# Kernel optimization log

Measured on AMD Instinct MI355X. Metric: run time of the kernel, lower is better.

## Reference

```python
import jax, jax.numpy as jnp
import numpy as np

LMAX, MMAX = 4, 2
K = (LMAX + 1) ** 2                                 # 25 SH coefficients (l-major node layout)
NL = [LMAX - m + 1 for m in range(MMAX + 1)]        # coeffs per order m: [5,4,3]
M_COEFF = NL[0] + sum(2 * n for n in NL[1:])        # 19 coeffs in m-major (mmax-truncated) edge layout
SPHERE_C, HIDDEN_C = 64, 64
NUM_HEADS, ALPHA_C, VALUE_C, OUT_C = 8, 32, 16, 64
P_GRID = 100
N_NODES, N_EDGES = 4096, 24576
NUM_SPECIES, EDGE_C, EMB_C = 90, 64, 64
N_EXTRA = NUM_HEADS * ALPHA_C + HIDDEN_C            # extra m=0 channels for S2_SEP: alpha + gate scalars


def _ln(x, g, b, eps=1e-5):
    mu = jnp.mean(x, -1, keepdims=True)
    var = jnp.var(x, -1, keepdims=True)
    return (x - mu) * jax.lax.rsqrt(var + eps) * g + b


def _smooth_leaky_relu(x, neg=0.2):
    return 0.5 * (1.0 + neg) * x + 0.5 * (1.0 - neg) * x * (2.0 * jax.nn.sigmoid(x) - 1.0)


def _segment_softmax(a, seg, n):
    amax = jax.lax.stop_gradient(jax.ops.segment_max(a, seg, num_segments=n))
    amax = jnp.where(jnp.isfinite(amax), amax, 0.0)
    e = jnp.exp(a - amax[seg])
    s = jax.ops.segment_sum(e, seg, num_segments=n)
    return e / (s[seg] + 1e-16)


def _so2_conv(x, w0, b0, wms, c_in, c_out, x_edge=None, n_extra=0):
    # x: [E, M_COEFF, c_in] in m-major layout (m=0 block, then per m: real rows then imag rows)
    E = x.shape[0]
    L0 = NL[0]
    x0 = x[:, :L0, :].reshape(E, L0 * c_in)
    if x_edge is not None:
        x0 = x0 * x_edge[:, :L0 * c_in]
    y0 = x0 @ w0 + b0
    extra = None
    if n_extra:
        extra = y0[:, L0 * c_out:]
        y0 = y0[:, :L0 * c_out]
    outs = [y0.reshape(E, L0, c_out)]
    off, rad = L0, L0 * c_in
    for m in range(1, MMAX + 1):
        nl = NL[m]
        xr = x[:, off:off + nl, :]
        xi = x[:, off + nl:off + 2 * nl, :]
        if x_edge is not None:
            s = x_edge[:, rad:rad + nl * c_in].reshape(E, nl, c_in)
            xr, xi = xr * s, xi * s
        xr = xr.reshape(E, nl * c_in)
        xi = xi.reshape(E, nl * c_in)
        half = nl * c_out
        wa, wb = wms[m - 1][:, :half], wms[m - 1][:, half:]
        yr = (xr @ wa - xi @ wb).reshape(E, nl, c_out)  # complex block-matmul
        yi = (xr @ wb + xi @ wa).reshape(E, nl, c_out)
        outs.append(jnp.concatenate([yr, yi], axis=1))
        off += 2 * nl
        rad += nl * c_in
    return jnp.concatenate(outs, axis=1), extra


def setup_inputs():
    key = jax.random.key(0)
    ks = iter(jax.random.split(key, 48))
    def w(shape, fan_in):
        return jax.random.normal(next(ks), shape, jnp.float32) / np.sqrt(fan_in)
    inp = {}
    inp['node_feats'] = jax.random.normal(next(ks), (N_NODES, K, SPHERE_C), jnp.float32)
    inp['node_species'] = jax.random.randint(next(ks), (N_NODES,), 0, NUM_SPECIES)
    inp['edge_distances'] = jax.random.normal(next(ks), (N_EDGES, EDGE_C), jnp.float32)
    inp['senders'] = jax.random.randint(next(ks), (N_EDGES,), 0, N_NODES)
    inp['receivers'] = jax.random.randint(next(ks), (N_EDGES,), 0, N_NODES)
    inp['wigner'] = jax.random.normal(next(ks), (N_EDGES, M_COEFF, K), jnp.float32) / np.sqrt(K)
    inp['snd_emb'] = jax.random.normal(next(ks), (NUM_SPECIES, EMB_C), jnp.float32) * 0.001
    inp['rcv_emb'] = jax.random.normal(next(ks), (NUM_SPECIES, EMB_C), jnp.float32) * 0.001
    ec = EDGE_C + 2 * EMB_C                              # 192 after atom-edge embedding concat
    n_rad = 2 * SPHERE_C * (NL[0] + NL[1] + NL[2])       # 1536 per-edge scales for conv1
    inp['rad_w1'] = w((ec, 64), ec); inp['rad_b1'] = jnp.zeros((64,))
    inp['rad_g1'] = jnp.ones((64,)); inp['rad_be1'] = jnp.zeros((64,))
    inp['rad_w2'] = w((64, 64), 64); inp['rad_b2'] = jnp.zeros((64,))
    inp['rad_g2'] = jnp.ones((64,)); inp['rad_be2'] = jnp.zeros((64,))
    inp['rad_w3'] = w((64, n_rad), 64); inp['rad_b3'] = jnp.ones((n_rad,))
    cin1 = 2 * SPHERE_C
    inp['c1_w0'] = w((NL[0] * cin1, NL[0] * HIDDEN_C + N_EXTRA), NL[0] * cin1)
    inp['c1_b0'] = jnp.zeros((NL[0] * HIDDEN_C + N_EXTRA,))
    inp['c1_wm1'] = w((NL[1] * cin1, 2 * NL[1] * HIDDEN_C), NL[1] * cin1)
    inp['c1_wm2'] = w((NL[2] * cin1, 2 * NL[2] * HIDDEN_C), NL[2] * cin1)
    inp['aln_g'] = jnp.ones((ALPHA_C,)); inp['aln_b'] = jnp.zeros((ALPHA_C,))
    inp['alpha_dot'] = w((NUM_HEADS, ALPHA_C), ALPHA_C)
    inp['to_grid'] = jax.random.normal(next(ks), (P_GRID, M_COEFF), jnp.float32) / np.sqrt(M_COEFF)
    inp['from_grid'] = jax.random.normal(next(ks), (M_COEFF, P_GRID), jnp.float32) / np.sqrt(P_GRID)
    cv = NUM_HEADS * VALUE_C
    inp['c2_w0'] = w((NL[0] * HIDDEN_C, NL[0] * cv), NL[0] * HIDDEN_C)
    inp['c2_b0'] = jnp.zeros((NL[0] * cv,))
    inp['c2_wm1'] = w((NL[1] * HIDDEN_C, 2 * NL[1] * cv), NL[1] * HIDDEN_C)
    inp['c2_wm2'] = w((NL[2] * HIDDEN_C, 2 * NL[2] * cv), NL[2] * HIDDEN_C)
    inp['proj_w'] = w((LMAX + 1, cv, OUT_C), cv)
    inp['proj_b'] = jnp.zeros((OUT_C,))
    return inp


def reference(node_feats, node_species, edge_distances, senders, receivers, wigner,
              snd_emb, rcv_emb, rad_w1, rad_b1, rad_g1, rad_be1, rad_w2, rad_b2,
              rad_g2, rad_be2, rad_w3, rad_b3, c1_w0, c1_b0, c1_wm1, c1_wm2,
              aln_g, aln_b, alpha_dot, to_grid, from_grid,
              c2_w0, c2_b0, c2_wm1, c2_wm2, proj_w, proj_b):
    N = node_feats.shape[0]
    # atom-edge embedding gathers + concat with radial-basis distances
    edge_embeds = jnp.concatenate([edge_distances,
                                   snd_emb[node_species[senders]],
                                   rcv_emb[node_species[receivers]]], axis=1)
    msgs = jnp.concatenate([node_feats[senders], node_feats[receivers]], axis=2)  # [E,25,128]
    msgs = jnp.einsum('emk,ekc->emc', wigner, msgs)                               # rotate to edge frame [E,19,128]
    # radial function -> per-edge input scales for SO2 conv 1
    h = jax.nn.silu(_ln(edge_embeds @ rad_w1 + rad_b1, rad_g1, rad_be1))
    h = jax.nn.silu(_ln(h @ rad_w2 + rad_b2, rad_g2, rad_be2))
    x_edge = h @ rad_w3 + rad_b3
    msgs, x0_extra = _so2_conv(msgs, c1_w0, c1_b0, [c1_wm1, c1_wm2],
                               2 * SPHERE_C, HIDDEN_C, x_edge, N_EXTRA)
    x0_alpha = x0_extra[:, :NUM_HEADS * ALPHA_C]
    x0_gate = x0_extra[:, NUM_HEADS * ALPHA_C:]
    # separable S2 activation: SiLU on sphere grid for l>0, SiLU on scalars for l=0
    grid = jax.nn.silu(jnp.einsum('pm,emc->epc', to_grid, msgs))
    tens = jnp.einsum('mp,epc->emc', from_grid, grid)
    msgs = jnp.concatenate([jax.nn.silu(x0_gate)[:, None, :], tens[:, 1:, :]], axis=1)
    msgs, _ = _so2_conv(msgs, c2_w0, c2_b0, [c2_wm1, c2_wm2], HIDDEN_C, NUM_HEADS * VALUE_C)
    # attention weights: LN -> SmoothLeakyReLU -> dot -> per-receiver softmax
    a = _smooth_leaky_relu(_ln(x0_alpha.reshape(-1, NUM_HEADS, ALPHA_C), aln_g, aln_b))
    alpha = _segment_softmax(jnp.einsum('ehk,hk->eh', a, alpha_dot), receivers, N)
    attn = msgs.reshape(-1, M_COEFF, NUM_HEADS, VALUE_C) * alpha[:, None, :, None]
    msgs = attn.reshape(-1, M_COEFF, NUM_HEADS * VALUE_C)
    msgs = jnp.einsum('emk,emc->ekc', wigner, msgs)    # rotate back (W^T), [E,25,128]
    node = jax.ops.segment_sum(msgs, receivers, num_segments=N)
    # SO3 linear: per-degree-l channel mixing, bias only on l=0
    l_of_k = jnp.asarray(np.repeat(np.arange(LMAX + 1), 2 * np.arange(LMAX + 1) + 1))
    out = jnp.einsum('nkc,kcd->nkd', node, proj_w[l_of_k])
    return out.at[:, 0, :].add(proj_b)
```

## Files before the change

### kernel.cpp

```cpp
#include <hip/hip_runtime.h>

typedef unsigned short u16;
typedef unsigned int u32;
typedef __attribute__((ext_vector_type(8))) short short8;
typedef __attribute__((ext_vector_type(4))) float floatx4;

#define E_EDGES 24576
#define EC 12288
#define N_NODES_C 4096

__device__ __forceinline__ float bf2f(u16 u) {
    union { u32 i; float f; } v; v.i = ((u32)u) << 16; return v.f;
}
__device__ __forceinline__ u16 f2bf(float f) {
    union { float f; u32 i; } v; v.f = f;
    u32 x = v.i;
    u32 r = (x + 0x7fffu + ((x >> 16) & 1u)) >> 16;
    return (u16)r;
}
__device__ __forceinline__ u32 pk_bf16(float a, float b) {
    u32 r;
    asm("v_cvt_pk_bf16_f32 %0, %1, %2" : "=v"(r) : "v"(a), "v"(b));
    return r;
}
__device__ __forceinline__ u32 encf(float f) {
    union { float f; u32 i; } v; v.f = f;
    return (v.i & 0x80000000u) ? ~v.i : (v.i | 0x80000000u);
}
__device__ __forceinline__ float decf(u32 u) {
    union { u32 i; float f; } v;
    v.i = (u & 0x80000000u) ? (u ^ 0x80000000u) : ~u;
    return v.f;
}
__device__ __forceinline__ float sigmoidf_(float x) { return __fdividef(1.f, 1.f + __expf(-x)); }
__device__ __forceinline__ float siluf_(float x) { return x * __fdividef(1.f, 1.f + __expf(-x)); }

__device__ __forceinline__ void gld16(const u16* g, u16* l) {
    __builtin_amdgcn_global_load_lds((const __attribute__((address_space(1))) unsigned int*)g,
                                     (__attribute__((address_space(3))) unsigned int*)l, 16, 0, 0);
}

__global__ void k_diag(float* __restrict__ out, int n) {
    int i = blockIdx.x * 256 + threadIdx.x;
    if (i < n) out[i] = 1000.0f;
}

__global__ void k_transpose(const float* __restrict__ src, u16* __restrict__ dst, int K, int N) {
    int idx = blockIdx.x * 256 + threadIdx.x;
    if (idx >= K * N) return;
    int k = idx / N, n = idx % N;
    dst[n * K + k] = f2bf(src[idx]);
}
__global__ void k_combine(const float* __restrict__ src, u16* __restrict__ dst, int K, int H) {
    int total = 4 * K * H;
    int idx = blockIdx.x * 256 + threadIdx.x;
    if (idx >= total) return;
    int n = idx / (2 * K), k = idx % (2 * K);
    float v;
    if (k < K) v = src[k * 2 * H + n];
    else {
        int kk = k - K;
        if (n < H) v = -src[kk * 2 * H + H + n];
        else       v = src[kk * 2 * H + (n - H)];
    }
    dst[idx] = f2bf(v);
}

__global__ void k_packgrid(const float* __restrict__ tg, const float* __restrict__ fg,
                           u16* __restrict__ tgP, u16* __restrict__ fgP) {
    int idx = blockIdx.x * 256 + threadIdx.x;
    if (idx < 112 * 32) {
        int p = idx >> 5, m = idx & 31;
        tgP[idx] = (p < 100 && m < 19) ? f2bf(tg[p * 19 + m]) : (u16)0;
    }
    int j = idx - 112 * 32;
    if (j >= 0 && j < 32 * 128) {
        int m = j >> 7, k = j & 127;
        fgP[j] = (m < 19 && k < 100) ? f2bf(fg[m * 100 + k]) : (u16)0;
    }
}

__global__ void k_init(u32* __restrict__ nmax, float* __restrict__ nsum, int n) {
    int idx = blockIdx.x * 256 + threadIdx.x;
    if (idx < n) { nmax[idx] = 0x007FFFFFu;  nsum[idx] = 0.f; }
}

__global__ void k_ee(const float* __restrict__ dist, const int* __restrict__ species,
                     const int* __restrict__ snd, const int* __restrict__ rcv,
                     const float* __restrict__ semb, const float* __restrict__ remb,
                     u16* __restrict__ ee) {
    int idx = blockIdx.x * 256 + threadIdx.x;
    if (idx >= E_EDGES * 192) return;
    int e = idx / 192, c = idx % 192;
    float v;
    if (c < 64)       v = dist[e * 64 + c];
    else if (c < 128) v = semb[species[snd[e]] * 64 + (c - 64)];
    else              v = remb[species[rcv[e]] * 64 + (c - 128)];
    ee[idx] = f2bf(v);
}

__global__ __launch_bounds__(256) void k_gemm(
    const u16* __restrict__ A, int lda,
    const u16* __restrict__ BT, int ldb,
    u16* __restrict__ C, int ldc,
    int N, int K,
    const float* __restrict__ bias) {
    __shared__ u16 As[128 * 32];
    __shared__ u16 Bs[128 * 32];
    int tid = threadIdx.x;
    int bm0 = blockIdx.x * 128;
    int bn0 = blockIdx.y * 128;
    int wave = tid >> 6, lane = tid & 63;
    int wm = (wave >> 1) * 64, wn = (wave & 1) * 64;
    int lrow = lane & 15, lk = (lane >> 4) * 8;

    int srow = (wave << 4) + (lane >> 2);
    int schunk = (lane & 3) << 3;
    const u16* Arow0 = A + (size_t)(bm0 + srow) * lda + schunk;
    const u16* Arow1 = A + (size_t)(bm0 + srow + 64) * lda + schunk;
    int n0 = bn0 + srow;      if (n0 >= N) n0 = N - 1;
    int n1 = bn0 + srow + 64; if (n1 >= N) n1 = N - 1;
    const u16* Brow0 = BT + (size_t)n0 * ldb + schunk;
    const u16* Brow1 = BT + (size_t)n1 * ldb + schunk;
    u16* lA0 = &As[srow * 32 + schunk];
    u16* lA1 = &As[(srow + 64) * 32 + schunk];
    u16* lB0 = &Bs[srow * 32 + schunk];
    u16* lB1 = &Bs[(srow + 64) * 32 + schunk];

    floatx4 acc[4][4];
#pragma unroll
    for (int i = 0; i < 4; i++)
#pragma unroll
        for (int j = 0; j < 4; j++) acc[i][j] = floatx4{0.f, 0.f, 0.f, 0.f};

    for (int k0 = 0; k0 < K; k0 += 32) {
        gld16(Arow0 + k0, lA0);
        gld16(Arow1 + k0, lA1);
        gld16(Brow0 + k0, lB0);
        gld16(Brow1 + k0, lB1);
        asm volatile("s_waitcnt vmcnt(0)" ::: "memory");
        __syncthreads();
        short8 a[4], b[4];
#pragma unroll
        for (int i = 0; i < 4; i++) a[i] = *(const short8*)(&As[(wm + i * 16 + lrow) * 32 + lk]);
#pragma unroll
        for (int j = 0; j < 4; j++) b[j] = *(const short8*)(&Bs[(wn + j * 16 + lrow) * 32 + lk]);
#pragma unroll
        for (int i = 0; i < 4; i++)
#pragma unroll
            for (int j = 0; j < 4; j++)
                acc[i][j] = __builtin_amdgcn_mfma_f32_16x16x32_bf16(a[i], b[j], acc[i][j], 0, 0, 0);
        __syncthreads();
    }

    int q = lane >> 4;
#pragma unroll
    for (int i = 0; i < 4; i++) {
#pragma unroll
        for (int j = 0; j < 4; j++) {
            int col = bn0 + wn + j * 16 + lrow;
            if (col < N) {
                float bv = bias ? bias[col] : 0.f;
#pragma unroll
                for (int r = 0; r < 4; r++) {
                    int row = bm0 + wm + i * 16 + q * 4 + r;
                    C[(size_t)row * ldc + col] = f2bf(acc[i][j][r] + bv);
                }
            }
        }
    }
}

__global__ __launch_bounds__(256) void k_ln_silu(const u16* __restrict__ in, u16* __restrict__ out,
                                                 const float* __restrict__ g, const float* __restrict__ b) {
    int tid = threadIdx.x;
    int e = blockIdx.x * 4 + (tid >> 6);
    int c = tid & 63;
    float x = bf2f(in[(size_t)e * 64 + c]);
    float s = x, s2 = x * x;
#pragma unroll
    for (int o = 32; o; o >>= 1) { s += __shfl_xor(s, o); s2 += __shfl_xor(s2, o); }
    float mu = s * (1.f / 64.f);
    float var = s2 * (1.f / 64.f) - mu * mu;
    float rs = rsqrtf(var + 1e-5f);
    float y = (x - mu) * rs * g[c] + b[c];
    out[(size_t)e * 64 + c] = f2bf(siluf_(y));
}

__global__ __launch_bounds__(256) void k_rotate(const float* __restrict__ nf, const float* __restrict__ wig,
                                                const int* __restrict__ snd, const int* __restrict__ rcv,
                                                const u16* __restrict__ xe, u16* __restrict__ A1, int e0) {
    __shared__ float wl[2][475];
    int tid = threadIdx.x;
    for (int i = tid; i < 950; i += 256) {
        int ee = e0 + blockIdx.x * 2 + (i / 475);
        wl[i / 475][i % 475] = wig[(size_t)ee * 475 + (i % 475)];
    }
    __syncthreads();
    int le = tid >> 7, c = tid & 127;
    int el = blockIdx.x * 2 + le;
    int e = e0 + el;
    int nd = (c < 64) ? snd[e] : rcv[e];
    int cc = c & 63;
    float msg[25];
#pragma unroll
    for (int k = 0; k < 25; k++) msg[k] = nf[(size_t)nd * 1600 + k * 64 + cc];
    const float* w = wl[le];
    size_t ebase = (size_t)el * 2432;
    size_t xbase = (size_t)el * 1536;
#pragma unroll
    for (int m = 0; m < 19; m++) {
        float r = 0.f;
#pragma unroll
        for (int k = 0; k < 25; k++) r += w[m * 25 + k] * msg[k];
        int a1c, xc;
        if (m < 5)       { a1c = m * 128;               xc = m * 128; }
        else if (m < 9)  { a1c = 640 + (m - 5) * 128;   xc = 640 + (m - 5) * 128; }
        else if (m < 13) { a1c = 1152 + (m - 9) * 128;  xc = 640 + (m - 9) * 128; }
        else if (m < 16) { a1c = 1664 + (m - 13) * 128; xc = 1152 + (m - 13) * 128; }
        else             { a1c = 2048 + (m - 16) * 128; xc = 1152 + (m - 16) * 128; }
        float sc = bf2f(xe[xbase + xc + c]);
        A1[ebase + a1c + c] = f2bf(r * sc);
    }
}

__global__ __launch_bounds__(256) void k_logits(const u16* __restrict__ Y0, const int* __restrict__ rcv,
                                                const float* __restrict__ g, const float* __restrict__ b,
                                                const float* __restrict__ adot,
                                                float* __restrict__ logits, u32* __restrict__ nmax) {
    int e = blockIdx.x;
    int tid = threadIdx.x;
    int h = tid >> 5, c = tid & 31;
    float x = bf2f(Y0[(size_t)e * 640 + 320 + h * 32 + c]);
    float s = x, s2 = x * x;
#pragma unroll
    for (int o = 16; o; o >>= 1) { s += __shfl_xor(s, o); s2 += __shfl_xor(s2, o); }
    float mu = s * (1.f / 32.f);
    float var = s2 * (1.f / 32.f) - mu * mu;
    float rs = rsqrtf(var + 1e-5f);
    float a = (x - mu) * rs * g[c] + b[c];
    float f = 0.6f * a + 0.4f * a * (2.f * sigmoidf_(a) - 1.f);
    float l = f * adot[h * 32 + c];
#pragma unroll
    for (int o = 16; o; o >>= 1) l += __shfl_xor(l, o);
    if (c == 0) {
        logits[e * 8 + h] = l;
        atomicMax(&nmax[rcv[e] * 8 + h], encf(l));
    }
}

__global__ void k_expsum(const float* __restrict__ logits, const int* __restrict__ rcv,
                         const u32* __restrict__ nmax, float* __restrict__ ealpha, float* __restrict__ nsum) {
    int idx = blockIdx.x * 256 + threadIdx.x;
    if (idx >= E_EDGES * 8) return;
    int e = idx >> 3, h = idx & 7;
    int r = rcv[e];
    float amax = decf(nmax[r * 8 + h]);
    if (!(amax > -1e38f && amax < 1e38f)) amax = 0.f;
    float v = __expf(logits[idx] - amax);
    ealpha[idx] = v;
    atomicAdd(&nsum[r * 8 + h], v);
}

#define GR_XS_STR 40
#define GR_T1_STR 136
__global__ __launch_bounds__(256) void k_grid_mfma(
    const u16* __restrict__ Y0, const u16* __restrict__ Y1, const u16* __restrict__ Y2,
    const u16* __restrict__ tgP, const u16* __restrict__ fgP, u16* __restrict__ A2) {
    __shared__ u16 Xs[128 * GR_XS_STR];
    __shared__ u16 T1s[128 * GR_T1_STR];
    int tid = threadIdx.x;
    int e0 = blockIdx.x * 2;
    {
        int row = tid >> 1;
        uint4 z = {0, 0, 0, 0};
        *(uint4*)(&T1s[row * GR_T1_STR + 112 + (tid & 1) * 8]) = z;
    }
    {
        int mp = tid & 15;
        int c0 = ((tid >> 4) & 7) << 3;
        int le = tid >> 7;
        int e = e0 + le;
        int m0 = 2 * mp, m1 = m0 + 1;
        uint4 va = {0, 0, 0, 0}, vb = {0, 0, 0, 0};
        if (m0 < 5)       va = *(const uint4*)(&Y0[(size_t)e * 640 + m0 * 64 + c0]);
        else if (m0 < 13) va = *(const uint4*)(&Y1[(size_t)e * 512 + (m0 - 5) * 64 + c0]);
        else if (m0 < 19) va = *(const uint4*)(&Y2[(size_t)e * 384 + (m0 - 13) * 64 + c0]);
        if (m1 < 5)       vb = *(const uint4*)(&Y0[(size_t)e * 640 + m1 * 64 + c0]);
        else if (m1 < 13) vb = *(const uint4*)(&Y1[(size_t)e * 512 + (m1 - 5) * 64 + c0]);
        else if (m1 < 19) vb = *(const uint4*)(&Y2[(size_t)e * 384 + (m1 - 13) * 64 + c0]);
        const u16* pa = (const u16*)&va;
        const u16* pb = (const u16*)&vb;
        int rbase = le * 64 + c0;
#pragma unroll
        for (int j = 0; j < 8; j++) {
            u32 w = (u32)pa[j] | ((u32)pb[j] << 16);
            *(u32*)(&Xs[(rbase + j) * GR_XS_STR + 2 * mp]) = w;
        }
    }
    __syncthreads();
    int wave = tid >> 6, lane = tid & 63;
    int wn = wave << 5;
    int ln = lane & 15, q = lane >> 4;
    short8 bx0 = *(const short8*)(&Xs[(wn + ln) * GR_XS_STR + q * 8]);
    short8 bx1 = *(const short8*)(&Xs[(wn + 16 + ln) * GR_XS_STR + q * 8]);
    floatx4 acc1[2][7];
#pragma unroll
    for (int pt = 0; pt < 7; pt++) {
        short8 a = *(const short8*)(&tgP[(size_t)(pt * 16 + ln) * 32 + q * 8]);
        acc1[0][pt] = __builtin_amdgcn_mfma_f32_16x16x32_bf16(a, bx0, floatx4{0.f, 0.f, 0.f, 0.f}, 0, 0, 0);
        acc1[1][pt] = __builtin_amdgcn_mfma_f32_16x16x32_bf16(a, bx1, floatx4{0.f, 0.f, 0.f, 0.f}, 0, 0, 0);
    }
#pragma unroll
    for (int i = 0; i < 2; i++) {
        u16* dst = &T1s[(wn + i * 16 + ln) * GR_T1_STR + q * 4];
#pragma unroll
        for (int pt = 0; pt < 7; pt++) {
            uint2 pv;
            pv.x = pk_bf16(siluf_(acc1[i][pt][0]), siluf_(acc1[i][pt][1]));
            pv.y = pk_bf16(siluf_(acc1[i][pt][2]), siluf_(acc1[i][pt][3]));
            *(uint2*)(dst + pt * 16) = pv;
        }
    }
    __syncthreads();
    floatx4 acc2[2][2];
    acc2[0][0] = floatx4{0.f, 0.f, 0.f, 0.f}; acc2[0][1] = floatx4{0.f, 0.f, 0.f, 0.f};
    acc2[1][0] = floatx4{0.f, 0.f, 0.f, 0.f}; acc2[1][1] = floatx4{0.f, 0.f, 0.f, 0.f};
#pragma unroll
    for (int ks = 0; ks < 4; ks++) {
        short8 c0 = *(const short8*)(&T1s[(wn + ln) * GR_T1_STR + ks * 32 + q * 8]);
        short8 c1 = *(const short8*)(&T1s[(wn + 16 + ln) * GR_T1_STR + ks * 32 + q * 8]);
#pragma unroll
        for (int ct = 0; ct < 2; ct++) {
            short8 b = *(const short8*)(&fgP[(size_t)(ct * 16 + ln) * 128 + ks * 32 + q * 8]);
            acc2[0][ct] = __builtin_amdgcn_mfma_f32_16x16x32_bf16(c0, b, acc2[0][ct], 0, 0, 0);
            acc2[1][ct] = __builtin_amdgcn_mfma_f32_16x16x32_bf16(c1, b, acc2[1][ct], 0, 0, 0);
        }
    }
#pragma unroll
    for (int rt = 0; rt < 2; rt++) {
        int row = wn + rt * 16 + q * 4;
        int e = e0 + (row >> 6), c = row & 63;
#pragma unroll
        for (int ct = 0; ct < 2; ct++) {
            int mp = ct * 16 + ln;
            if (mp >= 1 && mp < 19) {
                uint2 pv;
                pv.x = pk_bf16(acc2[rt][ct][0], acc2[rt][ct][1]);
                pv.y = pk_bf16(acc2[rt][ct][2], acc2[rt][ct][3]);
                *(uint2*)(&A2[(size_t)e * 1216 + mp * 64 + c]) = pv;
            }
        }
    }
    if (tid < 128) {
        int e = e0 + (tid >> 6), c = tid & 63;
        float gate = bf2f(Y0[(size_t)e * 640 + 576 + c]);
        A2[(size_t)e * 1216 + c] = f2bf(siluf_(gate));
    }
}

__global__ __launch_bounds__(256) void k_scatter(const u16* __restrict__ Z0, const u16* __restrict__ Z1,
                                                 const u16* __restrict__ Z2, const float* __restrict__ wig,
                                                 const float* __restrict__ ealpha, const float* __restrict__ nsum,
                                                 const int* __restrict__ rcv, float* __restrict__ node, int e0) {
    __shared__ float wl[2][475];
    int tid = threadIdx.x;
    for (int i = tid; i < 950; i += 256) {
        int ee = e0 + blockIdx.x * 2 + (i / 475);
        wl[i / 475][i % 475] = wig[(size_t)ee * 475 + (i % 475)];
    }
    __syncthreads();
    int le = tid >> 7, c = tid & 127;
    int el = blockIdx.x * 2 + le;
    int e = e0 + el;
    int r = rcv[e];
    int h = c >> 4;
    float al = ealpha[e * 8 + h] / (nsum[r * 8 + h] + 1e-16f);
    float s[19];
#pragma unroll
    for (int m = 0; m < 19; m++) {
        float v;
        if (m < 5)       v = bf2f(Z0[(size_t)el * 640 + m * 128 + c]);
        else if (m < 13) v = bf2f(Z1[(size_t)el * 1024 + (m - 5) * 128 + c]);
        else             v = bf2f(Z2[(size_t)el * 768 + (m - 13) * 128 + c]);
        s[m] = v * al;
    }
    const float* w = wl[le];
    float* nb = node + (size_t)r * 3200 + c;
#pragma unroll
    for (int k = 0; k < 25; k++) {
        float acc = 0.f;
#pragma unroll
        for (int m = 0; m < 19; m++) acc += w[m * 25 + k] * s[m];
        atomicAdd(&nb[k * 128], acc);
    }
}

#define PJ_STR 136
__global__ __launch_bounds__(256) void k_proj_mfma(
    const float* __restrict__ node, const u16* __restrict__ pwTb,
    const float* __restrict__ pb, float* __restrict__ out) {
    __shared__ u16 As[128 * PJ_STR];
    __shared__ u16 Bs[64 * PJ_STR];
    int tid = threadIdx.x;
    int n0 = blockIdx.x * 128;
    int k = blockIdx.y;
    int l = (int)sqrtf((float)k + 0.5f);
#pragma unroll
    for (int it = 0; it < 16; it++) {
        int i = tid + it * 256;
        int row = i >> 5;
        int c0 = (i & 31) << 2;
        float4 v = *(const float4*)(&node[(size_t)(n0 + row) * 3200 + k * 128 + c0]);
        uint2 pv;
        pv.x = pk_bf16(v.x, v.y);
        pv.y = pk_bf16(v.z, v.w);
        *(uint2*)(&As[row * PJ_STR + c0]) = pv;
    }
    const u16* pw = pwTb + (size_t)l * 8192;
#pragma unroll
    for (int jt = 0; jt < 4; jt++) {
        int j = tid + jt * 256;
        int d = j >> 4;
        int c0 = (j & 15) << 3;
        *(uint4*)(&Bs[d * PJ_STR + c0]) = *(const uint4*)(&pw[d * 128 + c0]);
    }
    __syncthreads();
    int wave = tid >> 6, lane = tid & 63;
    int wr = wave * 32;
    int ln = lane & 15, q = lane >> 4;
    floatx4 acc[2][4];
#pragma unroll
    for (int i = 0; i < 2; i++)
#pragma unroll
        for (int j = 0; j < 4; j++) acc[i][j] = floatx4{0.f, 0.f, 0.f, 0.f};
#pragma unroll
    for (int ks = 0; ks < 4; ks++) {
        short8 a0 = *(const short8*)(&As[(wr + ln) * PJ_STR + ks * 32 + q * 8]);
        short8 a1 = *(const short8*)(&As[(wr + 16 + ln) * PJ_STR + ks * 32 + q * 8]);
#pragma unroll
        for (int j = 0; j < 4; j++) {
            short8 b = *(const short8*)(&Bs[(j * 16 + ln) * PJ_STR + ks * 32 + q * 8]);
            acc[0][j] = __builtin_amdgcn_mfma_f32_16x16x32_bf16(a0, b, acc[0][j], 0, 0, 0);
            acc[1][j] = __builtin_amdgcn_mfma_f32_16x16x32_bf16(a1, b, acc[1][j], 0, 0, 0);
        }
    }
#pragma unroll
    for (int rt = 0; rt < 2; rt++)
#pragma unroll
        for (int j = 0; j < 4; j++) {
            int d = j * 16 + ln;
            float bv = (k == 0) ? pb[d] : 0.f;
#pragma unroll
            for (int r = 0; r < 4; r++) {
                int n = n0 + wr + rt * 16 + q * 4 + r;
                out[(size_t)n * 1600 + k * 64 + d] = acc[rt][j][r] + bv;
            }
        }
}

extern "C" void kernel_launch(void* const* d_in, const int* in_sizes, int n_in,
                              void* d_out, int out_size, void* d_ws, size_t ws_size,
                              hipStream_t stream) {
    const float* nf      = (const float*)d_in[0];
    const int* species   = (const int*)d_in[1];
    const float* dist    = (const float*)d_in[2];
    const int* snd       = (const int*)d_in[3];
    const int* rcv       = (const int*)d_in[4];
    const float* wig     = (const float*)d_in[5];
    const float* semb    = (const float*)d_in[6];
    const float* remb    = (const float*)d_in[7];
    const float* rad_w1  = (const float*)d_in[8];
    const float* rad_b1  = (const float*)d_in[9];
    const float* rad_g1  = (const float*)d_in[10];
    const float* rad_be1 = (const float*)d_in[11];
    const float* rad_w2  = (const float*)d_in[12];
    const float* rad_b2  = (const float*)d_in[13];
    const float* rad_g2  = (const float*)d_in[14];
    const float* rad_be2 = (const float*)d_in[15];
    const float* rad_w3  = (const float*)d_in[16];
    const float* rad_b3  = (const float*)d_in[17];
    const float* c1_w0   = (const float*)d_in[18];
    const float* c1_b0   = (const float*)d_in[19];
    const float* c1_wm1  = (const float*)d_in[20];
    const float* c1_wm2  = (const float*)d_in[21];
    const float* aln_g   = (const float*)d_in[22];
    const float* aln_b   = (const float*)d_in[23];
    const float* adot    = (const float*)d_in[24];
    const float* to_grid = (const float*)d_in[25];
    const float* from_grid=(const float*)d_in[26];
    const float* c2_w0   = (const float*)d_in[27];
    const float* c2_b0   = (const float*)d_in[28];
    const float* c2_wm1  = (const float*)d_in[29];
    const float* c2_wm2  = (const float*)d_in[30];
    const float* proj_w  = (const float*)d_in[31];
    const float* proj_b  = (const float*)d_in[32];

    char* ws = (char*)d_ws;
    size_t off = 0;
    auto take = [&](size_t bytes) -> char* {
        char* p = ws + off;
        off += (bytes + 255) & ~(size_t)255;
        return p;
    };
    u16* w_rad1T  = (u16*)take(64 * 192 * 2);
    u16* w_rad2T  = (u16*)take(64 * 64 * 2);
    u16* w_rad3T  = (u16*)take(1536 * 64 * 2);
    u16* w_c1w0T  = (u16*)take(640 * 640 * 2);
    u16* w_c1m1T  = (u16*)take((size_t)512 * 1024 * 2);
    u16* w_c1m2T  = (u16*)take((size_t)384 * 768 * 2);
    u16* w_c2w0T  = (u16*)take((size_t)640 * 320 * 2);
    u16* w_c2m1T  = (u16*)take((size_t)1024 * 512 * 2);
    u16* w_c2m2T  = (u16*)take((size_t)768 * 384 * 2);
    u16* w_tgP    = (u16*)take(112 * 32 * 2);
    u16* w_fgP    = (u16*)take(32 * 128 * 2);
    u16* w_pwT    = (u16*)take(5 * 8192 * 2);
    float* logits = (float*)take((size_t)E_EDGES * 8 * 4);
    float* ealpha = (float*)take((size_t)E_EDGES * 8 * 4);
    u32* nmax     = (u32*)take((size_t)N_NODES_C * 8 * 4);
    float* nsum   = (float*)take((size_t)N_NODES_C * 8 * 4);
    float* node   = (float*)take((size_t)N_NODES_C * 3200 * 4);
    u16* a_h2     = (u16*)take((size_t)E_EDGES * 64 * 2);
    char* arena   = take(173015040);
    if (off > ws_size) {
        k_diag<<<(out_size + 255) / 256, 256, 0, stream>>>((float*)d_out, out_size);
        return;
    }

    u16* a_ee   = (u16*)(arena + 0);
    u16* a_ypre = (u16*)(arena + 9437184);
    u16* a_h1   = (u16*)(arena + 12582912);
    u16* a_xe   = (u16*)(arena + 0);
    u16* a_A1   = (u16*)(arena + 37748736);
    u16* a_Y0   = (u16*)(arena + 97517568);
    u16* a_Y1   = (u16*)(arena + 128974848);
    u16* a_Y2   = (u16*)(arena + 154140672);
    u16* a_A2   = (u16*)(arena + 0);
    u16* a_Z0   = (u16*)(arena + 59768832);
    u16* a_Z1   = (u16*)(arena + 75497472);
    u16* a_Z2   = (u16*)(arena + 100663296);

    k_transpose<<<48, 256, 0, stream>>>(rad_w1, w_rad1T, 192, 64);
    k_transpose<<<16, 256, 0, stream>>>(rad_w2, w_rad2T, 64, 64);
    k_transpose<<<384, 256, 0, stream>>>(rad_w3, w_rad3T, 64, 1536);
    k_transpose<<<1600, 256, 0, stream>>>(c1_w0, w_c1w0T, 640, 640);
    k_transpose<<<800, 256, 0, stream>>>(c2_w0, w_c2w0T, 320, 640);
    k_combine<<<2048, 256, 0, stream>>>(c1_wm1, w_c1m1T, 512, 256);
    k_combine<<<1152, 256, 0, stream>>>(c1_wm2, w_c1m2T, 384, 192);
    k_combine<<<2048, 256, 0, stream>>>(c2_wm1, w_c2m1T, 256, 512);
    k_combine<<<1152, 256, 0, stream>>>(c2_wm2, w_c2m2T, 192, 384);
    k_packgrid<<<30, 256, 0, stream>>>(to_grid, from_grid, w_tgP, w_fgP);
    for (int l = 0; l < 5; l++)
        k_transpose<<<32, 256, 0, stream>>>(proj_w + (size_t)l * 8192, w_pwT + (size_t)l * 8192, 128, 64);
    k_init<<<128, 256, 0, stream>>>(nmax, nsum, N_NODES_C * 8);
    hipMemsetAsync(node, 0, (size_t)N_NODES_C * 3200 * 4, stream);

    k_ee<<<(E_EDGES * 192 + 255) / 256, 256, 0, stream>>>(dist, species, snd, rcv, semb, remb, a_ee);
    k_gemm<<<dim3(192, 1), 256, 0, stream>>>(a_ee, 192, w_rad1T, 192, a_ypre, 64, 64, 192, rad_b1);
    k_ln_silu<<<6144, 256, 0, stream>>>(a_ypre, a_h1, rad_g1, rad_be1);
    k_gemm<<<dim3(192, 1), 256, 0, stream>>>(a_h1, 64, w_rad2T, 64, a_ypre, 64, 64, 64, rad_b2);
    k_ln_silu<<<6144, 256, 0, stream>>>(a_ypre, a_h2, rad_g2, rad_be2);

    for (int c = 0; c < 2; c++) {
        int e0 = c * EC;
        k_gemm<<<dim3(96, 12), 256, 0, stream>>>(a_h2 + (size_t)e0 * 64, 64, w_rad3T, 64,
                                                 a_xe, 1536, 1536, 64, rad_b3);
        k_rotate<<<EC / 2, 256, 0, stream>>>(nf, wig, snd, rcv, a_xe, a_A1, e0);
        k_gemm<<<dim3(96, 5), 256, 0, stream>>>(a_A1, 2432, w_c1w0T, 640,
                                                a_Y0 + (size_t)e0 * 640, 640, 640, 640, c1_b0);
        k_gemm<<<dim3(96, 4), 256, 0, stream>>>(a_A1 + 640, 2432, w_c1m1T, 1024,
                                                a_Y1 + (size_t)e0 * 512, 512, 512, 1024, nullptr);
        k_gemm<<<dim3(96, 3), 256, 0, stream>>>(a_A1 + 1664, 2432, w_c1m2T, 768,
                                                a_Y2 + (size_t)e0 * 384, 384, 384, 768, nullptr);
    }

    k_logits<<<E_EDGES, 256, 0, stream>>>(a_Y0, rcv, aln_g, aln_b, adot, logits, nmax);
    k_expsum<<<(E_EDGES * 8 + 255) / 256, 256, 0, stream>>>(logits, rcv, nmax, ealpha, nsum);

    k_grid_mfma<<<E_EDGES / 2, 256, 0, stream>>>(a_Y0, a_Y1, a_Y2, w_tgP, w_fgP, a_A2);

    for (int c = 0; c < 2; c++) {
        int e0 = c * EC;
        k_gemm<<<dim3(96, 5), 256, 0, stream>>>(a_A2 + (size_t)e0 * 1216, 1216, w_c2w0T, 320,
                                                a_Z0, 640, 640, 320, c2_b0);
        k_gemm<<<dim3(96, 8), 256, 0, stream>>>(a_A2 + (size_t)e0 * 1216 + 320, 1216, w_c2m1T, 512,
                                                a_Z1, 1024, 1024, 512, nullptr);
        k_gemm<<<dim3(96, 6), 256, 0, stream>>>(a_A2 + (size_t)e0 * 1216 + 832, 1216, w_c2m2T, 384,
                                                a_Z2, 768, 768, 384, nullptr);
        k_scatter<<<EC / 2, 256, 0, stream>>>(a_Z0, a_Z1, a_Z2, wig, ealpha, nsum, rcv, node, e0);
    }

    k_proj_mfma<<<dim3(32, 25), 256, 0, stream>>>(node, w_pwT, proj_b, (float*)d_out);
}
```

Before: 1.072 ms.

## Replace atomic edge scatter with CSR-based per-node gather reduction

Builds a receiver-sorted edge list (degree count, prefix scan, fill) and replaces the per-edge atomicAdd scatter into node features with a per-node gather kernel that accumulates in registers and writes once. This removes 25 atomics per thread per edge and the memset of the node buffer. In exchange it adds three small setup kernels, irregular per-node work with load imbalance, Wigner coefficients read from global memory per thread instead of LDS, and the second chunk does a read-modify-write of node rows.

```diff
diff --git a/kernel.cpp b/kernel.cpp
--- a/kernel.cpp
+++ b/kernel.cpp
@@ -83,6 +83,34 @@
 __global__ void k_init(u32* __restrict__ nmax, float* __restrict__ nsum, int n) {
     int idx = blockIdx.x * 256 + threadIdx.x;
     if (idx < n) { nmax[idx] = 0x007FFFFFu;  nsum[idx] = 0.f; }
+}
+
+__global__ void k_deg(const int* __restrict__ rcv, u32* __restrict__ deg) {
+    int e = blockIdx.x * 256 + threadIdx.x;
+    if (e < E_EDGES) atomicAdd(&deg[rcv[e]], 1u);
+}
+__global__ __launch_bounds__(256) void k_pfx(const u32* __restrict__ deg,
+                                             u32* __restrict__ rowstart, u32* __restrict__ cur) {
+    __shared__ u32 ps[256];
+    int t = threadIdx.x;
+    u32 loc[16]; u32 s = 0;
+#pragma unroll
+    for (int i = 0; i < 16; i++) { loc[i] = s; s += deg[t * 16 + i]; }
+    ps[t] = s;
+    __syncthreads();
+    for (int o = 1; o < 256; o <<= 1) {
+        u32 v = (t >= o) ? ps[t - o] : 0u;
+        __syncthreads();
+        ps[t] += v;
+        __syncthreads();
+    }
+    u32 base = (t == 0) ? 0u : ps[t - 1];
+#pragma unroll
+    for (int i = 0; i < 16; i++) { u32 v = base + loc[i]; rowstart[t * 16 + i] = v; cur[t * 16 + i] = v; }
+}
+__global__ void k_fill(const int* __restrict__ rcv, u32* __restrict__ cur, int* __restrict__ elist) {
+    int e = blockIdx.x * 256 + threadIdx.x;
+    if (e < E_EDGES) { u32 p = atomicAdd(&cur[rcv[e]], 1u); elist[p] = e; }
 }
 
 __global__ void k_ee(const float* __restrict__ dist, const int* __restrict__ species,
@@ -359,40 +387,50 @@
     }
 }
 
-__global__ __launch_bounds__(256) void k_scatter(const u16* __restrict__ Z0, const u16* __restrict__ Z1,
-                                                 const u16* __restrict__ Z2, const float* __restrict__ wig,
-                                                 const float* __restrict__ ealpha, const float* __restrict__ nsum,
-                                                 const int* __restrict__ rcv, float* __restrict__ node, int e0) {
-    __shared__ float wl[2][475];
+__global__ __launch_bounds__(128) void k_gather(
+    const u16* __restrict__ Z0, const u16* __restrict__ Z1, const u16* __restrict__ Z2,
+    const float* __restrict__ wig, const float* __restrict__ ealpha, const float* __restrict__ nsum,
+    const u32* __restrict__ rowstart, const u32* __restrict__ deg, const int* __restrict__ elist,
+    float* __restrict__ node, int e0, int accum) {
+    int n = blockIdx.x;
     int tid = threadIdx.x;
-    for (int i = tid; i < 950; i += 256) {
-        int ee = e0 + blockIdx.x * 2 + (i / 475);
-        wl[i / 475][i % 475] = wig[(size_t)ee * 475 + (i % 475)];
-    }
-    __syncthreads();
-    int le = tid >> 7, c = tid & 127;
-    int el = blockIdx.x * 2 + le;
-    int e = e0 + el;
-    int r = rcv[e];
-    int h = c >> 4;
-    float al = ealpha[e * 8 + h] / (nsum[r * 8 + h] + 1e-16f);
-    float s[19];
-#pragma unroll
-    for (int m = 0; m < 19; m++) {
-        float v;
-        if (m < 5)       v = bf2f(Z0[(size_t)el * 640 + m * 128 + c]);
-        else if (m < 13) v = bf2f(Z1[(size_t)el * 1024 + (m - 5) * 128 + c]);
-        else             v = bf2f(Z2[(size_t)el * 768 + (m - 13) * 128 + c]);
-        s[m] = v * al;
-    }
-    const float* w = wl[le];
-    float* nb = node + (size_t)r * 3200 + c;
-#pragma unroll
-    for (int k = 0; k < 25; k++) {
-        float acc = 0.f;
-#pragma unroll
-        for (int m = 0; m < 19; m++) acc += w[m * 25 + k] * s[m];
-        atomicAdd(&nb[k * 128], acc);
+    int h = tid >> 4;
+    float acc[25];
+#pragma unroll
+    for (int k = 0; k < 25; k++) acc[k] = 0.f;
+    float sden = __fdividef(1.f, nsum[n * 8 + h] + 1e-16f);
+    u32 lo = rowstart[n], hi = lo + deg[n];
+    bool did = false;
+    for (u32 idx = lo; idx < hi; ++idx) {
+        int e = __builtin_amdgcn_readfirstlane(elist[idx]);
+        int el = e - e0;
+        if ((u32)el >= (u32)EC) continue;
+        did = true;
+        const float* w = wig + (size_t)e * 475;
+        float al = ealpha[e * 8 + h] * sden;
+        float s[19];
+#pragma unroll
+        for (int m = 0; m < 19; m++) {
+            float v;
+            if (m < 5)       v = bf2f(Z0[(size_t)el * 640 + m * 128 + tid]);
+            else if (m < 13) v = bf2f(Z1[(size_t)el * 1024 + (m - 5) * 128 + tid]);
+            else             v = bf2f(Z2[(size_t)el * 768 + (m - 13) * 128 + tid]);
+            s[m] = v * al;
+        }
+#pragma unroll
+        for (int m = 0; m < 19; m++)
+#pragma unroll
+            for (int k = 0; k < 25; k++)
+                acc[k] = fmaf(w[m * 25 + k], s[m], acc[k]);
+    }
+    float* nb = node + (size_t)n * 3200 + tid;
+    if (accum) {
+        if (!did) return;
+#pragma unroll
+        for (int k = 0; k < 25; k++) nb[k * 128] += acc[k];
+    } else {
+#pragma unroll
+        for (int k = 0; k < 25; k++) nb[k * 128] = acc[k];
     }
 }
 
@@ -521,6 +559,10 @@
     float* nsum   = (float*)take((size_t)N_NODES_C * 8 * 4);
     float* node   = (float*)take((size_t)N_NODES_C * 3200 * 4);
     u16* a_h2     = (u16*)take((size_t)E_EDGES * 64 * 2);
+    u32* c_deg    = (u32*)take((size_t)N_NODES_C * 4);
+    u32* c_row    = (u32*)take((size_t)N_NODES_C * 4);
+    u32* c_cur    = (u32*)take((size_t)N_NODES_C * 4);
+    int* c_elist  = (int*)take((size_t)E_EDGES * 4);
     char* arena   = take(173015040);
     if (off > ws_size) {
         k_diag<<<(out_size + 255) / 256, 256, 0, stream>>>((float*)d_out, out_size);
@@ -553,7 +595,11 @@
     for (int l = 0; l < 5; l++)
         k_transpose<<<32, 256, 0, stream>>>(proj_w + (size_t)l * 8192, w_pwT + (size_t)l * 8192, 128, 64);
     k_init<<<128, 256, 0, stream>>>(nmax, nsum, N_NODES_C * 8);
-    hipMemsetAsync(node, 0, (size_t)N_NODES_C * 3200 * 4, stream);
+
+    hipMemsetAsync(c_deg, 0, (size_t)N_NODES_C * 4, stream);
+    k_deg<<<96, 256, 0, stream>>>(rcv, c_deg);
+    k_pfx<<<1, 256, 0, stream>>>(c_deg, c_row, c_cur);
+    k_fill<<<96, 256, 0, stream>>>(rcv, c_cur, c_elist);
 
     k_ee<<<(E_EDGES * 192 + 255) / 256, 256, 0, stream>>>(dist, species, snd, rcv, semb, remb, a_ee);
     k_gemm<<<dim3(192, 1), 256, 0, stream>>>(a_ee, 192, w_rad1T, 192, a_ypre, 64, 64, 192, rad_b1);
@@ -587,7 +633,8 @@
                                                 a_Z1, 1024, 1024, 512, nullptr);
         k_gemm<<<dim3(96, 6), 256, 0, stream>>>(a_A2 + (size_t)e0 * 1216 + 832, 1216, w_c2m2T, 384,
                                                 a_Z2, 768, 768, 384, nullptr);
-        k_scatter<<<EC / 2, 256, 0, stream>>>(a_Z0, a_Z1, a_Z2, wig, ealpha, nsum, rcv, node, e0);
+        k_gather<<<N_NODES_C, 128, 0, stream>>>(a_Z0, a_Z1, a_Z2, wig, ealpha, nsum,
+                                                c_row, c_deg, c_elist, node, e0, c);
     }
 
     k_proj_mfma<<<dim3(32, 25), 256, 0, stream>>>(node, w_pwT, proj_b, (float*)d_out);
```

Result: no change. 1.055 ms (-1.6%).
